# Kernel optimization log

Measured on AMD Instinct MI355X. Metric: run time of the kernel, lower is better.

The kernel has to match this reference:

```python
import jax, jax.numpy as jnp
import numpy as np

B, S, D = 8, 2048, 768
N_SPANS = 512
MAX_W = 30  # static max span width (inclusive width in tokens)
H = 100
NEG = -1e30


def setup_inputs() -> dict:
    key = jax.random.key(0)
    k1, k2, k3, k4, k5, k6 = jax.random.split(key, 6)
    seq_tensor = jax.random.normal(k1, (B, S, D), dtype=jnp.float32)
    starts = jax.random.randint(k2, (B, N_SPANS), 0, S - MAX_W)
    widths = jax.random.randint(k3, (B, N_SPANS), 1, MAX_W + 1)  # span length in [1, MAX_W]
    ends_excl = starts + widths  # exclusive end, as module expects
    span_indices = jnp.stack([starts, ends_excl], axis=-1).astype(jnp.int64)
    span_mask = (jax.random.uniform(k4, (B, N_SPANS)) > 0.1).astype(jnp.int32)
    att_w = jax.random.normal(k5, (D, 1), dtype=jnp.float32) / np.sqrt(D)
    att_b = jnp.zeros((1,), dtype=jnp.float32)
    ffnn_w = jax.random.normal(k6, (D, H), dtype=jnp.float32) / np.sqrt(D)
    ffnn_b = jnp.zeros((H,), dtype=jnp.float32)
    return {"seq_tensor": seq_tensor, "span_indices": span_indices, "span_mask": span_mask,
            "att_w": att_w, "att_b": att_b, "ffnn_w": ffnn_w, "ffnn_b": ffnn_b}


def reference(seq_tensor, span_indices, span_mask, att_w, att_b, ffnn_w, ffnn_b):
    # exclusive end -> inclusive end (span_end_is_exclusive=True)
    starts = span_indices[..., 0]
    ends = span_indices[..., 1] - 1
    widths = ends - starts  # inclusive width - 1, in [0, MAX_W-1]

    offsets = jnp.arange(MAX_W)  # [W]
    raw_idx = starts[..., None] + offsets  # [B, N, W]
    width_mask = offsets <= widths[..., None]  # [B, N, W]
    idx = jnp.where(width_mask, raw_idx, 0)

    # global attention logits over the sequence: [B, S]
    att_logits = (jnp.einsum('bsd,do->bso', seq_tensor, att_w) + att_b)[..., 0]

    # gather span token embeddings and logits: [B, N, W, D], [B, N, W]
    span_emb = jax.vmap(lambda seq, i: seq[i])(seq_tensor, idx)
    span_logits = jax.vmap(lambda lg, i: lg[i])(att_logits, idx)

    # masked softmax over span width
    span_logits = jnp.where(width_mask, span_logits, NEG)
    attn = jax.nn.softmax(span_logits, axis=-1)  # [B, N, W]

    attended = jnp.einsum('bnw,bnwd->bnd', attn, span_emb)  # [B, N, D]
    attended = attended * span_mask.astype(attended.dtype)[..., None]

    # FeedForward: 1 layer Linear + tanh (dropout=0)
    out = jnp.tanh(jnp.einsum('bnd,dh->bnh', attended, ffnn_w) + ffnn_b)
    return out
```

## Files before the change

kernel.cpp:

```cpp
#include <hip/hip_runtime.h>
#include <cstdint>
#include <cstddef>

#define NB 8
#define NS 2048
#define ND 768
#define NSP 512
#define MAXW 30
#define NH 100
#define LDP 104
#define NKS (ND / 32)

typedef __attribute__((ext_vector_type(8))) short short8;
typedef __attribute__((ext_vector_type(4))) float floatx4;

union U4S8 { uint4 v; short8 s8; unsigned u[4]; unsigned short us[8]; };

__device__ inline unsigned short f2bf(float f) {
    unsigned u = __float_as_uint(f);
    return (unsigned short)((u + 0x7fffu + ((u >> 16) & 1u)) >> 16);
}

__device__ inline void split2(float x0, float x1, unsigned& hi, unsigned& lo) {
    unsigned u0 = __float_as_uint(x0), u1 = __float_as_uint(x1);
    unsigned h0 = u0 & 0xFFFF0000u, h1 = u1 & 0xFFFF0000u;
    hi = (u0 >> 16) | h1;
    float r0 = x0 - __uint_as_float(h0);
    float r1 = x1 - __uint_as_float(h1);
    lo = (__float_as_uint(r0) >> 16) | (__float_as_uint(r1) & 0xFFFF0000u);
}

__global__ __launch_bounds__(256) void pack_b_kernel(
    const float* __restrict__ ffnn_w, const float* __restrict__ att_w,
    uint4* __restrict__ Bfrag)
{
    int ks = blockIdx.x;
    for (int idx = threadIdx.x; idx < 8 * 64; idx += 256) {
        int cf = idx >> 6, lane = idx & 63;
        int q = lane >> 4, r = lane & 15;
        int n = cf * 16 + r;
        U4S8 p;
#pragma unroll
        for (int j = 0; j < 8; j++) {
            int k = ks * 32 + q * 8 + j;
            float v = (n < NH) ? ffnn_w[(size_t)k * NH + n]
                               : (n == NH ? att_w[k] : 0.f);
            p.us[j] = f2bf(v);
        }
        Bfrag[(size_t)(ks * 8 + cf) * 64 + lane] = p.v;
    }
}

__global__ __launch_bounds__(256, 4) void proj_kernel(
    const float* __restrict__ seq, const uint4* __restrict__ Bfrag,
    float* __restrict__ P, float* __restrict__ Lg)
{
    const int t = threadIdx.x;
    const int wave = t >> 6, lane = t & 63;
    const int q = lane >> 4, r = lane & 15;
    const int cf0 = wave * 2;
    const int row0 = blockIdx.x * 16;

    floatx4 acc[2] = {{0.f, 0.f, 0.f, 0.f}, {0.f, 0.f, 0.f, 0.f}};

    const float* arow = seq + (size_t)(row0 + r) * ND + q * 8;
    const uint4* bptr = Bfrag + (size_t)cf0 * 64 + lane;

#pragma unroll 2
    for (int ks = 0; ks < NKS; ++ks) {
        float4 f0 = *(const float4*)(arow + ks * 32);
        float4 f1 = *(const float4*)(arow + ks * 32 + 4);
        U4S8 b0, b1;
        b0.v = bptr[(size_t)ks * 8 * 64];
        b1.v = bptr[(size_t)ks * 8 * 64 + 64];

        U4S8 hi, lo;
        split2(f0.x, f0.y, hi.u[0], lo.u[0]);
        split2(f0.z, f0.w, hi.u[1], lo.u[1]);
        split2(f1.x, f1.y, hi.u[2], lo.u[2]);
        split2(f1.z, f1.w, hi.u[3], lo.u[3]);

        acc[0] = __builtin_amdgcn_mfma_f32_16x16x32_bf16(hi.s8, b0.s8, acc[0], 0, 0, 0);
        acc[0] = __builtin_amdgcn_mfma_f32_16x16x32_bf16(lo.s8, b0.s8, acc[0], 0, 0, 0);
        acc[1] = __builtin_amdgcn_mfma_f32_16x16x32_bf16(hi.s8, b1.s8, acc[1], 0, 0, 0);
        acc[1] = __builtin_amdgcn_mfma_f32_16x16x32_bf16(lo.s8, b1.s8, acc[1], 0, 0, 0);
    }

#pragma unroll
    for (int c = 0; c < 2; ++c) {
        int col = (cf0 + c) * 16 + r;
        if (col < NH) {
#pragma unroll
            for (int reg = 0; reg < 4; ++reg)
                P[(size_t)(row0 + q * 4 + reg) * LDP + col] = acc[c][reg];
        } else if (col == NH) {
#pragma unroll
            for (int reg = 0; reg < 4; ++reg)
                Lg[row0 + q * 4 + reg] = acc[c][reg];
        }
    }
}

__global__ __launch_bounds__(256) void span_kernel(
    const int* __restrict__ span_idx, const int* __restrict__ span_mask,
    const float* __restrict__ P, const float* __restrict__ Lg,
    const float* __restrict__ ffnn_b, float* __restrict__ out)
{
    const int wave = threadIdx.x >> 6, lane = threadIdx.x & 63;
    const int gs = blockIdx.x * 4 + wave;
    const int b = gs / NSP;
    const int st = span_idx[2 * gs];
    int w = span_idx[2 * gs + 1] - st;
    w = max(1, min(w, MAXW));

    float lg = -1e30f;
    if (lane < w) lg = Lg[b * NS + st + lane];
    float mx = lg;
#pragma unroll
    for (int off = 32; off > 0; off >>= 1) mx = fmaxf(mx, __shfl_xor(mx, off));
    float e = (lane < w) ? __expf(lg - mx) : 0.f;
    float sum = e;
#pragma unroll
    for (int off = 32; off > 0; off >>= 1) sum += __shfl_xor(sum, off);
    float attn = e / sum;

    int cl = min(lane, 24);
    const float4* Pb4 = (const float4*)(P + ((size_t)b * NS + st) * LDP) + cl;
    float4 acc = {0.f, 0.f, 0.f, 0.f};
#pragma unroll
    for (int i = 0; i < MAXW; ++i) {
        float a = __shfl(attn, i);
        float4 v = Pb4[i * (LDP / 4)];
        acc.x += a * v.x; acc.y += a * v.y; acc.z += a * v.z; acc.w += a * v.w;
    }

    if (lane < 25) {
        float m = (float)span_mask[gs];
        float4 bias = ((const float4*)ffnn_b)[lane];
        float4 o;
        o.x = tanhf(m * acc.x + bias.x);
        o.y = tanhf(m * acc.y + bias.y);
        o.z = tanhf(m * acc.z + bias.z);
        o.w = tanhf(m * acc.w + bias.w);
        *(float4*)(out + (size_t)gs * NH + 4 * lane) = o;
    }
}

extern "C" void kernel_launch(void* const* d_in, const int* in_sizes, int n_in,
                              void* d_out, int out_size, void* d_ws, size_t ws_size,
                              hipStream_t stream) {
    const float* seq      = (const float*)d_in[0];
    const int*   span_idx = (const int*)d_in[1];
    const int*   span_msk = (const int*)d_in[2];
    const float* att_w    = (const float*)d_in[3];
    const float* ffnn_w   = (const float*)d_in[5];
    const float* ffnn_b   = (const float*)d_in[6];
    float* out = (float*)d_out;

    char* ws = (char*)d_ws;
    float* P     = (float*)ws;
    uint4* Bfrag = (uint4*)(ws + (size_t)NB * NS * LDP * 4);
    float* Lg    = (float*)(ws + (size_t)NB * NS * LDP * 4 + (size_t)NKS * 8 * 64 * 16);

    pack_b_kernel<<<NKS, 256, 0, stream>>>(ffnn_w, att_w, Bfrag);
    proj_kernel<<<(NB * NS) / 16, 256, 0, stream>>>(seq, Bfrag, P, Lg);
    span_kernel<<<(NB * NSP) / 4, 256, 0, stream>>>(span_idx, span_msk, P, Lg, ffnn_b, out);
}
```

Before: 127.9 us.

## Fuse pack, projection and span kernels into one persistent kernel with grid barriers

Result: slower. 175.6 us (+37.3%).

```diff
diff --git a/kernel.cpp b/kernel.cpp
--- a/kernel.cpp
+++ b/kernel.cpp
@@ -9,7 +9,11 @@
 #define MAXW 30
 #define NH 100
 #define LDP 104
-#define NKS (ND / 32)
+#define NKS 24
+#define NCF 7
+#define NBLK 256
+#define NTHR 512
+#define NWAVES (NBLK * NTHR / 64)
 
 typedef __attribute__((ext_vector_type(8))) short short8;
 typedef __attribute__((ext_vector_type(4))) float floatx4;
@@ -30,14 +34,95 @@
     lo = (__float_as_uint(r0) >> 16) | (__float_as_uint(r1) & 0xFFFF0000u);
 }
 
-__global__ __launch_bounds__(256) void pack_b_kernel(
-    const float* __restrict__ ffnn_w, const float* __restrict__ att_w,
-    uint4* __restrict__ Bfrag)
+__device__ inline void grid_barrier(int* cnt, int* flag) {
+    __syncthreads();
+    if (threadIdx.x == 0) {
+        __threadfence();
+        int old = __hip_atomic_fetch_add(cnt, 1, __ATOMIC_ACQ_REL, __HIP_MEMORY_SCOPE_AGENT);
+        if (old == NBLK - 1) {
+            __hip_atomic_store(flag, 1, __ATOMIC_RELEASE, __HIP_MEMORY_SCOPE_AGENT);
+        } else {
+            while (__hip_atomic_load(flag, __ATOMIC_ACQUIRE, __HIP_MEMORY_SCOPE_AGENT) == 0)
+                __builtin_amdgcn_s_sleep(4);
+        }
+        __threadfence();
+    }
+    __syncthreads();
+}
+
+template<int NF>
+__device__ inline void proj_job(int tile, int cf0, int lane, int q, int r,
+                                const float* __restrict__ seq,
+                                const uint4* __restrict__ Bfrag,
+                                float* __restrict__ P, float* __restrict__ Lg)
 {
-    int ks = blockIdx.x;
-    for (int idx = threadIdx.x; idx < 8 * 64; idx += 256) {
-        int cf = idx >> 6, lane = idx & 63;
-        int q = lane >> 4, r = lane & 15;
+    const int row0 = tile * 16;
+    const float4* a4 = (const float4*)(seq + (size_t)(row0 + r) * ND) + q * 2;
+    const uint4* bp = Bfrag + (size_t)cf0 * 64 + lane;
+
+    floatx4 acc[NF];
+#pragma unroll
+    for (int c = 0; c < NF; ++c) acc[c] = (floatx4){0.f, 0.f, 0.f, 0.f};
+
+    float4 A00 = a4[0], A01 = a4[1];
+    float4 A10 = a4[8], A11 = a4[9];
+    uint4 Bc[NF];
+#pragma unroll
+    for (int c = 0; c < NF; ++c) Bc[c] = bp[c * 64];
+
+    for (int ks = 0; ks < NKS; ++ks) {
+        const int pa = (ks + 2 < NKS ? ks + 2 : NKS - 1) * 8;
+        const size_t pb = (size_t)(ks + 1 < NKS ? ks + 1 : NKS - 1) * (NCF * 64);
+        float4 N0 = a4[pa], N1 = a4[pa + 1];
+        uint4 Bn[NF];
+#pragma unroll
+        for (int c = 0; c < NF; ++c) Bn[c] = bp[pb + c * 64];
+
+        U4S8 hi, lo;
+        split2(A00.x, A00.y, hi.u[0], lo.u[0]);
+        split2(A00.z, A00.w, hi.u[1], lo.u[1]);
+        split2(A01.x, A01.y, hi.u[2], lo.u[2]);
+        split2(A01.z, A01.w, hi.u[3], lo.u[3]);
+
+#pragma unroll
+        for (int c = 0; c < NF; ++c) {
+            U4S8 b; b.v = Bc[c];
+            acc[c] = __builtin_amdgcn_mfma_f32_16x16x32_bf16(hi.s8, b.s8, acc[c], 0, 0, 0);
+            acc[c] = __builtin_amdgcn_mfma_f32_16x16x32_bf16(lo.s8, b.s8, acc[c], 0, 0, 0);
+        }
+        A00 = A10; A01 = A11; A10 = N0; A11 = N1;
+#pragma unroll
+        for (int c = 0; c < NF; ++c) Bc[c] = Bn[c];
+    }
+
+#pragma unroll
+    for (int c = 0; c < NF; ++c) {
+        int col = (cf0 + c) * 16 + r;
+        if (col < NH) {
+#pragma unroll
+            for (int reg = 0; reg < 4; ++reg)
+                P[(size_t)(row0 + q * 4 + reg) * LDP + col] = acc[c][reg];
+        } else if (col == NH) {
+#pragma unroll
+            for (int reg = 0; reg < 4; ++reg)
+                Lg[row0 + q * 4 + reg] = acc[c][reg];
+        }
+    }
+}
+
+__global__ __launch_bounds__(NTHR) void fused_kernel(
+    const float* __restrict__ seq, const int* __restrict__ span_idx,
+    const int* __restrict__ span_mask, const float* __restrict__ att_w,
+    const float* __restrict__ ffnn_w, const float* __restrict__ ffnn_b,
+    float* __restrict__ out, float* __restrict__ P,
+    uint4* __restrict__ Bfrag, float* __restrict__ Lg, int* __restrict__ bar)
+{
+    const int wave = threadIdx.x >> 6, lane = threadIdx.x & 63;
+    const int q = lane >> 4, r = lane & 15;
+    const int wid = blockIdx.x * 8 + wave;
+
+    if (wid < NKS * NCF) {
+        int ks = wid / NCF, cf = wid - ks * NCF;
         int n = cf * 16 + r;
         U4S8 p;
 #pragma unroll
@@ -47,102 +132,56 @@
                                : (n == NH ? att_w[k] : 0.f);
             p.us[j] = f2bf(v);
         }
-        Bfrag[(size_t)(ks * 8 + cf) * 64 + lane] = p.v;
-    }
-}
-
-__global__ __launch_bounds__(256, 4) void proj_kernel(
-    const float* __restrict__ seq, const uint4* __restrict__ Bfrag,
-    float* __restrict__ P, float* __restrict__ Lg)
-{
-    const int t = threadIdx.x;
-    const int wave = t >> 6, lane = t & 63;
-    const int q = lane >> 4, r = lane & 15;
-    const int cf0 = wave * 2;
-    const int row0 = blockIdx.x * 16;
-
-    floatx4 acc[2] = {{0.f, 0.f, 0.f, 0.f}, {0.f, 0.f, 0.f, 0.f}};
-
-    const float* arow = seq + (size_t)(row0 + r) * ND + q * 8;
-    const uint4* bptr = Bfrag + (size_t)cf0 * 64 + lane;
-
-#pragma unroll 2
-    for (int ks = 0; ks < NKS; ++ks) {
-        float4 f0 = *(const float4*)(arow + ks * 32);
-        float4 f1 = *(const float4*)(arow + ks * 32 + 4);
-        U4S8 b0, b1;
-        b0.v = bptr[(size_t)ks * 8 * 64];
-        b1.v = bptr[(size_t)ks * 8 * 64 + 64];
-
-        U4S8 hi, lo;
-        split2(f0.x, f0.y, hi.u[0], lo.u[0]);
-        split2(f0.z, f0.w, hi.u[1], lo.u[1]);
-        split2(f1.x, f1.y, hi.u[2], lo.u[2]);
-        split2(f1.z, f1.w, hi.u[3], lo.u[3]);
-
-        acc[0] = __builtin_amdgcn_mfma_f32_16x16x32_bf16(hi.s8, b0.s8, acc[0], 0, 0, 0);
-        acc[0] = __builtin_amdgcn_mfma_f32_16x16x32_bf16(lo.s8, b0.s8, acc[0], 0, 0, 0);
-        acc[1] = __builtin_amdgcn_mfma_f32_16x16x32_bf16(hi.s8, b1.s8, acc[1], 0, 0, 0);
-        acc[1] = __builtin_amdgcn_mfma_f32_16x16x32_bf16(lo.s8, b1.s8, acc[1], 0, 0, 0);
-    }
-
-#pragma unroll
-    for (int c = 0; c < 2; ++c) {
-        int col = (cf0 + c) * 16 + r;
-        if (col < NH) {
-#pragma unroll
-            for (int reg = 0; reg < 4; ++reg)
-                P[(size_t)(row0 + q * 4 + reg) * LDP + col] = acc[c][reg];
-        } else if (col == NH) {
-#pragma unroll
-            for (int reg = 0; reg < 4; ++reg)
-                Lg[row0 + q * 4 + reg] = acc[c][reg];
-        }
-    }
-}
-
-__global__ __launch_bounds__(256) void span_kernel(
-    const int* __restrict__ span_idx, const int* __restrict__ span_mask,
-    const float* __restrict__ P, const float* __restrict__ Lg,
-    const float* __restrict__ ffnn_b, float* __restrict__ out)
-{
-    const int wave = threadIdx.x >> 6, lane = threadIdx.x & 63;
-    const int gs = blockIdx.x * 4 + wave;
-    const int b = gs / NSP;
-    const int st = span_idx[2 * gs];
-    int w = span_idx[2 * gs + 1] - st;
-    w = max(1, min(w, MAXW));
-
-    float lg = -1e30f;
-    if (lane < w) lg = Lg[b * NS + st + lane];
-    float mx = lg;
-#pragma unroll
-    for (int off = 32; off > 0; off >>= 1) mx = fmaxf(mx, __shfl_xor(mx, off));
-    float e = (lane < w) ? __expf(lg - mx) : 0.f;
-    float sum = e;
-#pragma unroll
-    for (int off = 32; off > 0; off >>= 1) sum += __shfl_xor(sum, off);
-    float attn = e / sum;
-
-    int cl = min(lane, 24);
-    const float4* Pb4 = (const float4*)(P + ((size_t)b * NS + st) * LDP) + cl;
-    float4 acc = {0.f, 0.f, 0.f, 0.f};
-#pragma unroll
-    for (int i = 0; i < MAXW; ++i) {
-        float a = __shfl(attn, i);
-        float4 v = Pb4[i * (LDP / 4)];
-        acc.x += a * v.x; acc.y += a * v.y; acc.z += a * v.z; acc.w += a * v.w;
-    }
-
-    if (lane < 25) {
-        float m = (float)span_mask[gs];
-        float4 bias = ((const float4*)ffnn_b)[lane];
-        float4 o;
-        o.x = tanhf(m * acc.x + bias.x);
-        o.y = tanhf(m * acc.y + bias.y);
-        o.z = tanhf(m * acc.z + bias.z);
-        o.w = tanhf(m * acc.w + bias.w);
-        *(float4*)(out + (size_t)gs * NH + 4 * lane) = o;
+        Bfrag[(size_t)wid * 64 + lane] = p.v;
+    }
+    grid_barrier(bar + 0, bar + 1);
+
+    {
+        const int tile = wid >> 1, half = wid & 1;
+        if (half == 0) proj_job<4>(tile, 0, lane, q, r, seq, Bfrag, P, Lg);
+        else           proj_job<3>(tile, 4, lane, q, r, seq, Bfrag, P, Lg);
+    }
+    grid_barrier(bar + 2, bar + 3);
+
+#pragma unroll
+    for (int j = 0; j < 2; ++j) {
+        const int gs = wid + j * NWAVES;
+        const int b = gs / NSP;
+        const int st = span_idx[2 * gs];
+        int w = span_idx[2 * gs + 1] - st;
+        w = max(1, min(w, MAXW));
+
+        float lg = -1e30f;
+        if (lane < w) lg = Lg[b * NS + st + lane];
+        float mx = lg;
+#pragma unroll
+        for (int off = 32; off > 0; off >>= 1) mx = fmaxf(mx, __shfl_xor(mx, off));
+        float e = (lane < w) ? __expf(lg - mx) : 0.f;
+        float sum = e;
+#pragma unroll
+        for (int off = 32; off > 0; off >>= 1) sum += __shfl_xor(sum, off);
+        float attn = e / sum;
+
+        int cl = min(lane, 24);
+        const float4* Pb4 = (const float4*)(P + ((size_t)b * NS + st) * LDP) + cl;
+        float4 acc = {0.f, 0.f, 0.f, 0.f};
+#pragma unroll
+        for (int i = 0; i < MAXW; ++i) {
+            float a = __shfl(attn, i);
+            float4 v = Pb4[i * (LDP / 4)];
+            acc.x += a * v.x; acc.y += a * v.y; acc.z += a * v.z; acc.w += a * v.w;
+        }
+
+        if (lane < 25) {
+            float m = (float)span_mask[gs];
+            float4 bias = ((const float4*)ffnn_b)[lane];
+            float4 o;
+            o.x = tanhf(m * acc.x + bias.x);
+            o.y = tanhf(m * acc.y + bias.y);
+            o.z = tanhf(m * acc.z + bias.z);
+            o.w = tanhf(m * acc.w + bias.w);
+            *(float4*)(out + (size_t)gs * NH + 4 * lane) = o;
+        }
     }
 }
 
@@ -158,11 +197,14 @@
     float* out = (float*)d_out;
 
     char* ws = (char*)d_ws;
-    float* P     = (float*)ws;
-    uint4* Bfrag = (uint4*)(ws + (size_t)NB * NS * LDP * 4);
-    float* Lg    = (float*)(ws + (size_t)NB * NS * LDP * 4 + (size_t)NKS * 8 * 64 * 16);
-
-    pack_b_kernel<<<NKS, 256, 0, stream>>>(ffnn_w, att_w, Bfrag);
-    proj_kernel<<<(NB * NS) / 16, 256, 0, stream>>>(seq, Bfrag, P, Lg);
-    span_kernel<<<(NB * NSP) / 4, 256, 0, stream>>>(span_idx, span_msk, P, Lg, ffnn_b, out);
-}
+    size_t off = 0;
+    float* P     = (float*)(ws + off); off += (size_t)NB * NS * LDP * 4;
+    uint4* Bfrag = (uint4*)(ws + off); off += (size_t)NKS * NCF * 64 * 16;
+    float* Lg    = (float*)(ws + off); off += (size_t)NB * NS * 4;
+    int*   bar   = (int*)(ws + ((off + 255) & ~(size_t)255));
+
+    hipMemsetAsync(bar, 0, 256, stream);
+
+    fused_kernel<<<NBLK, NTHR, 0, stream>>>(
+        seq, span_idx, span_msk, att_w, ffnn_w, ffnn_b, out, P, Bfrag, Lg, bar);
+}
```

## Use one wave per column fragment, drop padded fragment, prefetch next k-chunk

Applied to the files above, without the earlier changes.

Measured after the change: 140.7 us. 1.1x slower.

```diff
diff --git a/kernel.cpp b/kernel.cpp
--- a/kernel.cpp
+++ b/kernel.cpp
@@ -9,7 +9,8 @@
 #define MAXW 30
 #define NH 100
 #define LDP 104
-#define NKS (ND / 32)
+#define NKS 24
+#define NCF 7
 
 typedef __attribute__((ext_vector_type(8))) short short8;
 typedef __attribute__((ext_vector_type(4))) float floatx4;
@@ -35,7 +36,7 @@
     uint4* __restrict__ Bfrag)
 {
     int ks = blockIdx.x;
-    for (int idx = threadIdx.x; idx < 8 * 64; idx += 256) {
+    for (int idx = threadIdx.x; idx < NCF * 64; idx += 256) {
         int cf = idx >> 6, lane = idx & 63;
         int q = lane >> 4, r = lane & 15;
         int n = cf * 16 + r;
@@ -47,57 +48,63 @@
                                : (n == NH ? att_w[k] : 0.f);
             p.us[j] = f2bf(v);
         }
-        Bfrag[(size_t)(ks * 8 + cf) * 64 + lane] = p.v;
+        Bfrag[(size_t)(ks * NCF + cf) * 64 + lane] = p.v;
     }
 }
 
-__global__ __launch_bounds__(256, 4) void proj_kernel(
+__global__ __launch_bounds__(448, 6) void proj_kernel(
     const float* __restrict__ seq, const uint4* __restrict__ Bfrag,
     float* __restrict__ P, float* __restrict__ Lg)
 {
-    const int t = threadIdx.x;
-    const int wave = t >> 6, lane = t & 63;
+    const int cf = threadIdx.x >> 6, lane = threadIdx.x & 63;
     const int q = lane >> 4, r = lane & 15;
-    const int cf0 = wave * 2;
     const int row0 = blockIdx.x * 16;
 
-    floatx4 acc[2] = {{0.f, 0.f, 0.f, 0.f}, {0.f, 0.f, 0.f, 0.f}};
+    const float4* a4 = (const float4*)(seq + (size_t)(row0 + r) * ND) + q * 2;
+    const uint4* bp = Bfrag + (size_t)cf * 64 + lane;
 
-    const float* arow = seq + (size_t)(row0 + r) * ND + q * 8;
-    const uint4* bptr = Bfrag + (size_t)cf0 * 64 + lane;
+    floatx4 acc = {0.f, 0.f, 0.f, 0.f};
 
-#pragma unroll 2
-    for (int ks = 0; ks < NKS; ++ks) {
-        float4 f0 = *(const float4*)(arow + ks * 32);
-        float4 f1 = *(const float4*)(arow + ks * 32 + 4);
-        U4S8 b0, b1;
-        b0.v = bptr[(size_t)ks * 8 * 64];
-        b1.v = bptr[(size_t)ks * 8 * 64 + 64];
+    float4 A0 = a4[0], A1 = a4[1], A2 = a4[8], A3 = a4[9];
+    uint4  B0 = bp[0], B1 = bp[448];
 
-        U4S8 hi, lo;
-        split2(f0.x, f0.y, hi.u[0], lo.u[0]);
-        split2(f0.z, f0.w, hi.u[1], lo.u[1]);
-        split2(f1.x, f1.y, hi.u[2], lo.u[2]);
-        split2(f1.z, f1.w, hi.u[3], lo.u[3]);
+    for (int c = 0; c < NKS / 2; ++c) {
+        const int nc = (c + 1 < NKS / 2) ? c + 1 : c;
+        const int na = nc * 16;
+        const size_t nb = (size_t)nc * 2 * 448;
+        float4 N0 = a4[na], N1 = a4[na + 1], N2 = a4[na + 8], N3 = a4[na + 9];
+        uint4  M0 = bp[nb], M1 = bp[nb + 448];
 
-        acc[0] = __builtin_amdgcn_mfma_f32_16x16x32_bf16(hi.s8, b0.s8, acc[0], 0, 0, 0);
-        acc[0] = __builtin_amdgcn_mfma_f32_16x16x32_bf16(lo.s8, b0.s8, acc[0], 0, 0, 0);
-        acc[1] = __builtin_amdgcn_mfma_f32_16x16x32_bf16(hi.s8, b1.s8, acc[1], 0, 0, 0);
-        acc[1] = __builtin_amdgcn_mfma_f32_16x16x32_bf16(lo.s8, b1.s8, acc[1], 0, 0, 0);
+        U4S8 hi, lo, b;
+        split2(A0.x, A0.y, hi.u[0], lo.u[0]);
+        split2(A0.z, A0.w, hi.u[1], lo.u[1]);
+        split2(A1.x, A1.y, hi.u[2], lo.u[2]);
+        split2(A1.z, A1.w, hi.u[3], lo.u[3]);
+        b.v = B0;
+        acc = __builtin_amdgcn_mfma_f32_16x16x32_bf16(hi.s8, b.s8, acc, 0, 0, 0);
+        acc = __builtin_amdgcn_mfma_f32_16x16x32_bf16(lo.s8, b.s8, acc, 0, 0, 0);
+
+        split2(A2.x, A2.y, hi.u[0], lo.u[0]);
+        split2(A2.z, A2.w, hi.u[1], lo.u[1]);
+        split2(A3.x, A3.y, hi.u[2], lo.u[2]);
+        split2(A3.z, A3.w, hi.u[3], lo.u[3]);
+        b.v = B1;
+        acc = __builtin_amdgcn_mfma_f32_16x16x32_bf16(hi.s8, b.s8, acc, 0, 0, 0);
+        acc = __builtin_amdgcn_mfma_f32_16x16x32_bf16(lo.s8, b.s8, acc, 0, 0, 0);
+
+        A0 = N0; A1 = N1; A2 = N2; A3 = N3;
+        B0 = M0; B1 = M1;
     }
 
+    const int col = cf * 16 + r;
+    if (col < NH) {
 #pragma unroll
-    for (int c = 0; c < 2; ++c) {
-        int col = (cf0 + c) * 16 + r;
-        if (col < NH) {
+        for (int reg = 0; reg < 4; ++reg)
+            P[(size_t)(row0 + q * 4 + reg) * LDP + col] = acc[reg];
+    } else if (col == NH) {
 #pragma unroll
-            for (int reg = 0; reg < 4; ++reg)
-                P[(size_t)(row0 + q * 4 + reg) * LDP + col] = acc[c][reg];
-        } else if (col == NH) {
-#pragma unroll
-            for (int reg = 0; reg < 4; ++reg)
-                Lg[row0 + q * 4 + reg] = acc[c][reg];
-        }
+        for (int reg = 0; reg < 4; ++reg)
+            Lg[row0 + q * 4 + reg] = acc[reg];
     }
 }
 
@@ -158,11 +165,12 @@
     float* out = (float*)d_out;
 
     char* ws = (char*)d_ws;
-    float* P     = (float*)ws;
-    uint4* Bfrag = (uint4*)(ws + (size_t)NB * NS * LDP * 4);
-    float* Lg    = (float*)(ws + (size_t)NB * NS * LDP * 4 + (size_t)NKS * 8 * 64 * 16);
+    size_t off = 0;
+    float* P     = (float*)(ws + off); off += (size_t)NB * NS * LDP * 4;
+    uint4* Bfrag = (uint4*)(ws + off); off += (size_t)NKS * NCF * 64 * 16;
+    float* Lg    = (float*)(ws + off);
 
     pack_b_kernel<<<NKS, 256, 0, stream>>>(ffnn_w, att_w, Bfrag);
-    proj_kernel<<<(NB * NS) / 16, 256, 0, stream>>>(seq, Bfrag, P, Lg);
+    proj_kernel<<<(NB * NS) / 16, 448, 0, stream>>>(seq, Bfrag, P, Lg);
     span_kernel<<<(NB * NSP) / 4, 256, 0, stream>>>(span_idx, span_msk, P, Lg, ffnn_b, out);
 }
```

## Stage seq tiles through LDS with 32-row blocks and register prefetch

Applied to the files above, without the earlier changes.

Measured after the change: 118.5 us. 1.08x faster.

```diff
diff --git a/kernel.cpp b/kernel.cpp
--- a/kernel.cpp
+++ b/kernel.cpp
@@ -9,7 +9,11 @@
 #define MAXW 30
 #define NH 100
 #define LDP 104
-#define NKS (ND / 32)
+#define NKS 24
+#define NCF 8
+#define BM 32
+#define BKF 64
+#define NIT 12
 
 typedef __attribute__((ext_vector_type(8))) short short8;
 typedef __attribute__((ext_vector_type(4))) float floatx4;
@@ -35,7 +39,7 @@
     uint4* __restrict__ Bfrag)
 {
     int ks = blockIdx.x;
-    for (int idx = threadIdx.x; idx < 8 * 64; idx += 256) {
+    for (int idx = threadIdx.x; idx < NCF * 64; idx += 256) {
         int cf = idx >> 6, lane = idx & 63;
         int q = lane >> 4, r = lane & 15;
         int n = cf * 16 + r;
@@ -47,56 +51,81 @@
                                : (n == NH ? att_w[k] : 0.f);
             p.us[j] = f2bf(v);
         }
-        Bfrag[(size_t)(ks * 8 + cf) * 64 + lane] = p.v;
+        Bfrag[(size_t)(ks * NCF + cf) * 64 + lane] = p.v;
     }
 }
 
-__global__ __launch_bounds__(256, 4) void proj_kernel(
+__global__ __launch_bounds__(256) void proj_kernel(
     const float* __restrict__ seq, const uint4* __restrict__ Bfrag,
     float* __restrict__ P, float* __restrict__ Lg)
 {
+    __shared__ float As[BM][BKF + 4];
     const int t = threadIdx.x;
     const int wave = t >> 6, lane = t & 63;
     const int q = lane >> 4, r = lane & 15;
-    const int cf0 = wave * 2;
-    const int row0 = blockIdx.x * 16;
+    const int wr = wave & 1, wc = wave >> 1;
+    const int cf0 = wc * 4;
+    const int row0 = blockIdx.x * BM;
 
-    floatx4 acc[2] = {{0.f, 0.f, 0.f, 0.f}, {0.f, 0.f, 0.f, 0.f}};
+    floatx4 acc[4] = {{0.f,0.f,0.f,0.f},{0.f,0.f,0.f,0.f},
+                      {0.f,0.f,0.f,0.f},{0.f,0.f,0.f,0.f}};
 
-    const float* arow = seq + (size_t)(row0 + r) * ND + q * 8;
-    const uint4* bptr = Bfrag + (size_t)cf0 * 64 + lane;
+    const int sr = t >> 4, sc = t & 15;
+    const float4* gA0 = (const float4*)(seq + (size_t)(row0 + sr) * ND);
+    const float4* gA1 = (const float4*)(seq + (size_t)(row0 + 16 + sr) * ND);
+    float* w0 = &As[sr][sc * 4];
+    float* w1 = &As[16 + sr][sc * 4];
 
-#pragma unroll 2
-    for (int ks = 0; ks < NKS; ++ks) {
-        float4 f0 = *(const float4*)(arow + ks * 32);
-        float4 f1 = *(const float4*)(arow + ks * 32 + 4);
-        U4S8 b0, b1;
-        b0.v = bptr[(size_t)ks * 8 * 64];
-        b1.v = bptr[(size_t)ks * 8 * 64 + 64];
+    float4 s0 = gA0[sc], s1 = gA1[sc];
 
-        U4S8 hi, lo;
-        split2(f0.x, f0.y, hi.u[0], lo.u[0]);
-        split2(f0.z, f0.w, hi.u[1], lo.u[1]);
-        split2(f1.x, f1.y, hi.u[2], lo.u[2]);
-        split2(f1.z, f1.w, hi.u[3], lo.u[3]);
+    const float* rdbase = &As[wr * 16 + r][q * 8];
+    const uint4* bp = Bfrag + (size_t)cf0 * 64 + lane;
 
-        acc[0] = __builtin_amdgcn_mfma_f32_16x16x32_bf16(hi.s8, b0.s8, acc[0], 0, 0, 0);
-        acc[0] = __builtin_amdgcn_mfma_f32_16x16x32_bf16(lo.s8, b0.s8, acc[0], 0, 0, 0);
-        acc[1] = __builtin_amdgcn_mfma_f32_16x16x32_bf16(hi.s8, b1.s8, acc[1], 0, 0, 0);
-        acc[1] = __builtin_amdgcn_mfma_f32_16x16x32_bf16(lo.s8, b1.s8, acc[1], 0, 0, 0);
+    for (int i = 0; i < NIT; ++i) {
+        __syncthreads();
+        *(float4*)w0 = s0;
+        *(float4*)w1 = s1;
+        __syncthreads();
+        const int nx = (i + 1 < NIT ? i + 1 : i) * 16 + sc;
+        s0 = gA0[nx]; s1 = gA1[nx];
+
+        uint4 Bv[8];
+#pragma unroll
+        for (int ksl = 0; ksl < 2; ++ksl)
+#pragma unroll
+            for (int c = 0; c < 4; ++c)
+                Bv[ksl * 4 + c] = bp[(size_t)((i * 2 + ksl) * NCF) * 64 + c * 64];
+
+#pragma unroll
+        for (int ksl = 0; ksl < 2; ++ksl) {
+            float4 a0 = *(const float4*)(rdbase + ksl * 32);
+            float4 a1 = *(const float4*)(rdbase + ksl * 32 + 4);
+            U4S8 hi, lo;
+            split2(a0.x, a0.y, hi.u[0], lo.u[0]);
+            split2(a0.z, a0.w, hi.u[1], lo.u[1]);
+            split2(a1.x, a1.y, hi.u[2], lo.u[2]);
+            split2(a1.z, a1.w, hi.u[3], lo.u[3]);
+#pragma unroll
+            for (int c = 0; c < 4; ++c) {
+                U4S8 b; b.v = Bv[ksl * 4 + c];
+                acc[c] = __builtin_amdgcn_mfma_f32_16x16x32_bf16(hi.s8, b.s8, acc[c], 0, 0, 0);
+                acc[c] = __builtin_amdgcn_mfma_f32_16x16x32_bf16(lo.s8, b.s8, acc[c], 0, 0, 0);
+            }
+        }
     }
 
 #pragma unroll
-    for (int c = 0; c < 2; ++c) {
-        int col = (cf0 + c) * 16 + r;
+    for (int c = 0; c < 4; ++c) {
+        const int col = (cf0 + c) * 16 + r;
+        const int rowb = row0 + wr * 16 + q * 4;
         if (col < NH) {
 #pragma unroll
             for (int reg = 0; reg < 4; ++reg)
-                P[(size_t)(row0 + q * 4 + reg) * LDP + col] = acc[c][reg];
+                P[(size_t)(rowb + reg) * LDP + col] = acc[c][reg];
         } else if (col == NH) {
 #pragma unroll
             for (int reg = 0; reg < 4; ++reg)
-                Lg[row0 + q * 4 + reg] = acc[c][reg];
+                Lg[rowb + reg] = acc[c][reg];
         }
     }
 }
@@ -158,11 +187,12 @@
     float* out = (float*)d_out;
 
     char* ws = (char*)d_ws;
-    float* P     = (float*)ws;
-    uint4* Bfrag = (uint4*)(ws + (size_t)NB * NS * LDP * 4);
-    float* Lg    = (float*)(ws + (size_t)NB * NS * LDP * 4 + (size_t)NKS * 8 * 64 * 16);
+    size_t off = 0;
+    float* P     = (float*)(ws + off); off += (size_t)NB * NS * LDP * 4;
+    uint4* Bfrag = (uint4*)(ws + off); off += (size_t)NKS * NCF * 64 * 16;
+    float* Lg    = (float*)(ws + off);
 
     pack_b_kernel<<<NKS, 256, 0, stream>>>(ffnn_w, att_w, Bfrag);
-    proj_kernel<<<(NB * NS) / 16, 256, 0, stream>>>(seq, Bfrag, P, Lg);
+    proj_kernel<<<(NB * NS) / BM, 256, 0, stream>>>(seq, Bfrag, P, Lg);
     span_kernel<<<(NB * NSP) / 4, 256, 0, stream>>>(span_idx, span_msk, P, Lg, ffnn_b, out);
 }
```
